# Kernel tuning notes

Hardware: AMD Instinct MI355X
Metric: run time of the kernel (lower is better)

Reference implementation:

```python
import jax, jax.numpy as jnp
import numpy as np

B, T, D, HEADS = 4, 2048, 2048, 16  # math requires T == D


def setup_inputs() -> dict:
    key = jax.random.key(0)
    k1, k2, k3 = jax.random.split(key, 3)
    scale = 1.0 / np.sqrt(D)
    x = jax.random.normal(k1, (B, T, D), dtype=jnp.float32)
    w_qk = jax.random.normal(k2, (2 * D, D), dtype=jnp.float32) * scale
    w_dense = jax.random.normal(k3, (D, D), dtype=jnp.float32) * scale
    b_dense = jnp.zeros((D,), dtype=jnp.float32)
    return {"x": x, "w_qk": w_qk, "w_dense": w_dense, "b_dense": b_dense}


def reference(x, w_qk, w_dense, b_dense):
    b, t, d = x.shape
    h = HEADS
    vh = d // h
    # to_q_k: Linear(d, 2d, bias=False); chunk into k0, v
    kv = jnp.einsum('btd,ed->bte', x, w_qk)          # [b,t,2d]
    k0, v = kv[..., :d], kv[..., d:]                 # each [b,t,d]
    scale_factor = 1.0 / jnp.sqrt(jnp.asarray(d * (d - 1) / 2, dtype=x.dtype))
    # k = k0.transpose(1,2) -> [b,d,t]; scores = k @ v^T -> [b,d,t] (t==d)
    s = jnp.einsum('bmi,bjm->bij', k0, v) * scale_factor   # [b,d,t]
    a = jax.nn.softmax(s, axis=-1)
    q = jnp.einsum('bit,btd->bid', a, v)             # [b,d,d]
    # q.transpose(0,1).chunk(h, dim=0) -> stack(dim=1) -> transpose(1,2) -> reshape
    qt = jnp.swapaxes(q, 0, 1)                       # [d, b, d]
    stk = qt.reshape(h, vh, b, d)                    # h chunks of [vh,b,d]
    stk = jnp.transpose(stk, (1, 0, 2, 3))           # stack(dim=1): [vh,h,b,d]
    stk = jnp.transpose(stk, (0, 2, 1, 3))           # transpose(1,2): [vh,b,h,d]
    out = stk.reshape(b, t, d)
    # dropout in eval mode == identity; to_dense Linear
    return jnp.einsum('btd,ed->bte', out, w_dense) + b_dense
```

## Files before the change

### kernel.cpp

```cpp
#include <hip/hip_runtime.h>
#include <stdint.h>
#include <math.h>


typedef __bf16 bf16x8 __attribute__((ext_vector_type(8)));
typedef float  f32x4  __attribute__((ext_vector_type(4)));

__device__ __forceinline__ float bf2f(uint16_t u) {
  union { uint32_t i; float f; } c; c.i = ((uint32_t)u) << 16; return c.f;
}
__device__ __forceinline__ uint16_t f2bf(float f) {
  union { float f; uint32_t i; } c; c.f = f;
  uint32_t i = c.i;
  return (uint16_t)((i + 0x7fffu + ((i >> 16) & 1u)) >> 16);
}

__device__ __forceinline__ void gll16(const void* g, void* l) {
  __builtin_amdgcn_global_load_lds((const __attribute__((address_space(1))) void*)g,
                                   (__attribute__((address_space(3))) void*)l,
                                   16, 0, 0);
}

#define NX4 4194304u
#define NW4 2097152u
#define ND4 1048576u
__global__ __launch_bounds__(256) void k_cast_all(
    const float* __restrict__ x, const float* __restrict__ wqk,
    const float* __restrict__ wd, uint16_t* __restrict__ dst) {
  uint32_t i = blockIdx.x * 256 + threadIdx.x;
  float4 v;
  if (i < NX4)            v = reinterpret_cast<const float4*>(x)[i];
  else if (i < NX4 + NW4) v = reinterpret_cast<const float4*>(wqk)[i - NX4];
  else                    v = reinterpret_cast<const float4*>(wd)[i - NX4 - NW4];
  ushort4 o;
  o.x = f2bf(v.x); o.y = f2bf(v.y); o.z = f2bf(v.z); o.w = f2bf(v.w);
  reinterpret_cast<ushort4*>(dst)[i] = o;
}

__device__ __forceinline__ void gemm_core(
    const uint16_t* a0, const uint16_t* a1, const uint16_t* a2, const uint16_t* a3,
    const uint16_t* b0, const uint16_t* b1, const uint16_t* b2, const uint16_t* b3,
    uint16_t* As, uint16_t* Bs, int K, f32x4 acc[4][4])
{
  const int tid = threadIdx.x;
  const int w = tid >> 6, l = tid & 63;
  const int wm = (w >> 1) * 64, wn = (w & 1) * 64;
  const int frow = l & 15, fkc = l >> 4;
  const int xr = frow & 7;
  const int off0 = ((0 * 4 + fkc) ^ xr) * 8;
  const int off1 = ((1 * 4 + fkc) ^ xr) * 8;
  uint16_t* lA0 = As + 0 * 2048 + w * 512;
  uint16_t* lA1 = As + 1 * 2048 + w * 512;
  uint16_t* lA2 = As + 2 * 2048 + w * 512;
  uint16_t* lA3 = As + 3 * 2048 + w * 512;
  uint16_t* lB0 = Bs + 0 * 2048 + w * 512;
  uint16_t* lB1 = Bs + 1 * 2048 + w * 512;
  uint16_t* lB2 = Bs + 2 * 2048 + w * 512;
  uint16_t* lB3 = Bs + 3 * 2048 + w * 512;
  for (int kb = 0; kb < K; kb += 64) {
    __syncthreads();
    gll16(a0, lA0); gll16(a1, lA1); gll16(a2, lA2); gll16(a3, lA3);
    gll16(b0, lB0); gll16(b1, lB1); gll16(b2, lB2); gll16(b3, lB3);
    a0 += 64; a1 += 64; a2 += 64; a3 += 64;
    b0 += 64; b1 += 64; b2 += 64; b3 += 64;
    __syncthreads();
#pragma unroll
    for (int h = 0; h < 2; ++h) {
      const int off = h ? off1 : off0;
      bf16x8 af[4], bfv[4];
#pragma unroll
      for (int mi = 0; mi < 4; ++mi)
        af[mi] = *reinterpret_cast<const bf16x8*>(&As[(wm + mi * 16 + frow) * 64 + off]);
#pragma unroll
      for (int ni = 0; ni < 4; ++ni)
        bfv[ni] = *reinterpret_cast<const bf16x8*>(&Bs[(wn + ni * 16 + frow) * 64 + off]);
#pragma unroll
      for (int mi = 0; mi < 4; ++mi)
#pragma unroll
        for (int ni = 0; ni < 4; ++ni)
          acc[mi][ni] = __builtin_amdgcn_mfma_f32_16x16x32_bf16(af[mi], bfv[ni], acc[mi][ni], 0, 0, 0);
    }
  }
}

__device__ __forceinline__ const uint16_t* stage_ptr(
    const uint16_t* base, int tile_row0, int c, int lda) {
  const int tid = threadIdx.x;
  const int r3 = tid >> 3;
  const int ko = (((tid & 7) ^ (r3 & 7)) * 8);
  return base + (size_t)(tile_row0 + c * 32 + r3) * lda + ko;
}

__global__ __launch_bounds__(256) void k_gemm_kv(
    const uint16_t* __restrict__ W,
    const uint16_t* __restrict__ X,
    uint16_t* __restrict__ k0T,
    uint16_t* __restrict__ vT)
{
  __shared__ uint16_t As[8192], Bs[8192];
  const int bm = blockIdx.y, bn = blockIdx.x;
  f32x4 acc[4][4];
#pragma unroll
  for (int i = 0; i < 4; ++i)
#pragma unroll
    for (int j = 0; j < 4; ++j) acc[i][j] = (f32x4){0.f, 0.f, 0.f, 0.f};
  gemm_core(stage_ptr(W, bm * 128, 0, 2048), stage_ptr(W, bm * 128, 1, 2048),
            stage_ptr(W, bm * 128, 2, 2048), stage_ptr(W, bm * 128, 3, 2048),
            stage_ptr(X, bn * 128, 0, 2048), stage_ptr(X, bn * 128, 1, 2048),
            stage_ptr(X, bn * 128, 2, 2048), stage_ptr(X, bn * 128, 3, 2048),
            As, Bs, 2048, acc);
  const int tid = threadIdx.x;
  const int w = tid >> 6, l = tid & 63;
  const int wm = (w >> 1) * 64, wn = (w & 1) * 64;
  const int cr = (l >> 4) * 4, cc = l & 15;
  uint16_t* Cb = (bm < 16) ? (k0T + (size_t)bm * 128 * 8192)
                           : (vT + (size_t)(bm - 16) * 128 * 8192);
#pragma unroll
  for (int mi = 0; mi < 4; ++mi)
#pragma unroll
    for (int ni = 0; ni < 4; ++ni)
#pragma unroll
      for (int g = 0; g < 4; ++g) {
        int lr = wm + mi * 16 + cr + g;
        int bt = bn * 128 + wn + ni * 16 + cc;
        Cb[(size_t)lr * 8192 + bt] = f2bf(acc[mi][ni][g]);
      }
}

__global__ __launch_bounds__(256) void k_gemm_bt(
    const uint16_t* __restrict__ A, int lda, long sA,
    const uint16_t* __restrict__ B, int ldb, long sB,
    uint16_t* __restrict__ C, int ldc, long sC,
    int K, float scale)
{
  __shared__ uint16_t As[8192], Bs[8192];
  const int z = blockIdx.z;
  A += (size_t)z * sA; B += (size_t)z * sB; C += (size_t)z * sC;
  const int bm = blockIdx.y, bn = blockIdx.x;
  f32x4 acc[4][4];
#pragma unroll
  for (int i = 0; i < 4; ++i)
#pragma unroll
    for (int j = 0; j < 4; ++j) acc[i][j] = (f32x4){0.f, 0.f, 0.f, 0.f};
  gemm_core(stage_ptr(A, bm * 128, 0, lda), stage_ptr(A, bm * 128, 1, lda),
            stage_ptr(A, bm * 128, 2, lda), stage_ptr(A, bm * 128, 3, lda),
            stage_ptr(B, bn * 128, 0, ldb), stage_ptr(B, bn * 128, 1, ldb),
            stage_ptr(B, bn * 128, 2, ldb), stage_ptr(B, bn * 128, 3, ldb),
            As, Bs, K, acc);
  const int tid = threadIdx.x;
  const int w = tid >> 6, l = tid & 63;
  const int wm = (w >> 1) * 64, wn = (w & 1) * 64;
  const int cr = (l >> 4) * 4, cc = l & 15;
#pragma unroll
  for (int mi = 0; mi < 4; ++mi)
#pragma unroll
    for (int ni = 0; ni < 4; ++ni)
#pragma unroll
      for (int g = 0; g < 4; ++g) {
        int grow = bm * 128 + wm + mi * 16 + cr + g;
        int gcol = bn * 128 + wn + ni * 16 + cc;
        C[(size_t)grow * ldc + gcol] = f2bf(acc[mi][ni][g] * scale);
      }
}

__device__ __forceinline__ size_t qrow_off(int rr) {
  int bp = rr >> 11, tp = rr & 2047;
  int bi = (tp >> 4) & 3;
  int i  = (tp & 15) * 128 + bp * 32 + (tp >> 6);
  return ((size_t)bi * 2048 + (size_t)i) * 2048;
}

__global__ __launch_bounds__(256) void k_gemm_out(
    const uint16_t* __restrict__ Q,
    const uint16_t* __restrict__ W,
    const float*    __restrict__ bias,
    float*          __restrict__ Out)
{
  __shared__ uint16_t As[8192], Bs[8192];
  const int tid = threadIdx.x;
  const int bm = blockIdx.y, bn = blockIdx.x;
  const int r3 = tid >> 3;
  const int ko = (((tid & 7) ^ (r3 & 7)) * 8);
  const uint16_t* a0 = Q + qrow_off(bm * 128 + 0 * 32 + r3) + ko;
  const uint16_t* a1 = Q + qrow_off(bm * 128 + 1 * 32 + r3) + ko;
  const uint16_t* a2 = Q + qrow_off(bm * 128 + 2 * 32 + r3) + ko;
  const uint16_t* a3 = Q + qrow_off(bm * 128 + 3 * 32 + r3) + ko;
  f32x4 acc[4][4];
#pragma unroll
  for (int i = 0; i < 4; ++i)
#pragma unroll
    for (int j = 0; j < 4; ++j) acc[i][j] = (f32x4){0.f, 0.f, 0.f, 0.f};
  gemm_core(a0, a1, a2, a3,
            stage_ptr(W, bn * 128, 0, 2048), stage_ptr(W, bn * 128, 1, 2048),
            stage_ptr(W, bn * 128, 2, 2048), stage_ptr(W, bn * 128, 3, 2048),
            As, Bs, 2048, acc);
  const int w = tid >> 6, l = tid & 63;
  const int wm = (w >> 1) * 64, wn = (w & 1) * 64;
  const int cr = (l >> 4) * 4, cc = l & 15;
#pragma unroll
  for (int mi = 0; mi < 4; ++mi)
#pragma unroll
    for (int ni = 0; ni < 4; ++ni)
#pragma unroll
      for (int g = 0; g < 4; ++g) {
        int grow = bm * 128 + wm + mi * 16 + cr + g;
        int gcol = bn * 128 + wn + ni * 16 + cc;
        Out[(size_t)grow * 2048 + gcol] = acc[mi][ni][g] + bias[gcol];
      }
}

__global__ __launch_bounds__(256) void k_transpose(
    const uint16_t* __restrict__ src, uint16_t* __restrict__ dst)
{
  __shared__ uint16_t tile[64][65];
  const int tid = threadIdx.x;
  const int bx = blockIdx.x;
  const int by = blockIdx.y;
  const int cu = tid & 31, r0 = tid >> 5;
#pragma unroll
  for (int p = 0; p < 8; ++p) {
    int r = p * 8 + r0;
    uint32_t v = *reinterpret_cast<const uint32_t*>(
        &src[(size_t)(by * 64 + r) * 8192 + bx * 64 + cu * 2]);
    tile[r][cu * 2]     = (uint16_t)(v & 0xffffu);
    tile[r][cu * 2 + 1] = (uint16_t)(v >> 16);
  }
  __syncthreads();
#pragma unroll
  for (int p = 0; p < 8; ++p) {
    int r = p * 8 + r0;
    uint32_t lo = tile[cu * 2][r], hi = tile[cu * 2 + 1][r];
    *reinterpret_cast<uint32_t*>(
        &dst[(size_t)(bx * 64 + r) * 2048 + by * 64 + cu * 2]) = lo | (hi << 16);
  }
}

__global__ __launch_bounds__(256) void k_softmax(uint16_t* __restrict__ s)
{
  uint16_t* p = s + (size_t)blockIdx.x * 2048;
  const int tid = threadIdx.x;
  uint4 raw = reinterpret_cast<const uint4*>(p)[tid];
  uint32_t u[4] = {raw.x, raw.y, raw.z, raw.w};
  float x[8];
#pragma unroll
  for (int i = 0; i < 4; ++i) {
    x[2 * i]     = bf2f((uint16_t)(u[i] & 0xffffu));
    x[2 * i + 1] = bf2f((uint16_t)(u[i] >> 16));
  }
  float m = x[0];
#pragma unroll
  for (int i = 1; i < 8; ++i) m = fmaxf(m, x[i]);
#pragma unroll
  for (int o = 32; o; o >>= 1) m = fmaxf(m, __shfl_xor(m, o, 64));
  __shared__ float redm[4], reds[4];
  if ((tid & 63) == 0) redm[tid >> 6] = m;
  __syncthreads();
  m = fmaxf(fmaxf(redm[0], redm[1]), fmaxf(redm[2], redm[3]));
  float sum = 0.f;
#pragma unroll
  for (int i = 0; i < 8; ++i) { x[i] = __expf(x[i] - m); sum += x[i]; }
#pragma unroll
  for (int o = 32; o; o >>= 1) sum += __shfl_xor(sum, o, 64);
  if ((tid & 63) == 0) reds[tid >> 6] = sum;
  __syncthreads();
  sum = reds[0] + reds[1] + reds[2] + reds[3];
  float inv = 1.0f / sum;
  uint32_t ou[4];
#pragma unroll
  for (int i = 0; i < 4; ++i) {
    uint32_t lo = f2bf(x[2 * i] * inv);
    uint32_t hi = f2bf(x[2 * i + 1] * inv);
    ou[i] = lo | (hi << 16);
  }
  reinterpret_cast<uint4*>(p)[tid] = make_uint4(ou[0], ou[1], ou[2], ou[3]);
}

extern "C" void kernel_launch(void* const* d_in, const int* in_sizes, int n_in,
                              void* d_out, int out_size, void* d_ws, size_t ws_size,
                              hipStream_t stream) {
  const float* x       = (const float*)d_in[0];
  const float* w_qk    = (const float*)d_in[1];
  const float* w_dense = (const float*)d_in[2];
  const float* b_dense = (const float*)d_in[3];
  float* out = (float*)d_out;

  const size_t NX = 4ull * 2048 * 2048;
  const size_t NW = 4096ull * 2048;
  const size_t ND = 2048ull * 2048;

  uint16_t* xb   = (uint16_t*)d_ws;
  uint16_t* wqkb = xb + NX;
  uint16_t* wdb  = wqkb + NW;
  uint16_t* k0T  = wdb + ND;
  uint16_t* vT   = k0T + NX;
  uint16_t* qb   = xb;
  uint16_t* Vn   = (uint16_t*)d_out;
  uint16_t* sb   = Vn + NX;

  const float scale = (float)(1.0 / sqrt(0.5 * 2048.0 * 2047.0));

  k_cast_all<<<dim3((NX4 + NW4 + ND4) / 256), 256, 0, stream>>>(x, w_qk, w_dense, xb);

  k_gemm_kv<<<dim3(64, 32), 256, 0, stream>>>(wqkb, xb, k0T, vT);
  k_transpose<<<dim3(128, 32), 256, 0, stream>>>(vT, Vn);
  k_gemm_bt<<<dim3(16, 16, 4), 256, 0, stream>>>(
      k0T, 8192, 2048L, Vn, 2048, 2048L * 2048L, sb, 2048, 2048L * 2048L, 2048, scale);
  k_softmax<<<dim3(8192), 256, 0, stream>>>(sb);
  k_gemm_bt<<<dim3(16, 16, 4), 256, 0, stream>>>(
      sb, 2048, 2048L * 2048L, vT, 8192, 2048L, qb, 2048, 2048L * 2048L, 2048, 1.0f);
  k_gemm_out<<<dim3(16, 64), 256, 0, stream>>>(qb, wdb, b_dense, out);
}
```

Before: 575.9 us.

## Replace direct global-to-LDS loads with register-prefetched double staging in GEMM core

```diff
diff --git a/kernel.cpp b/kernel.cpp
--- a/kernel.cpp
+++ b/kernel.cpp
@@ -13,12 +13,6 @@
   union { float f; uint32_t i; } c; c.f = f;
   uint32_t i = c.i;
   return (uint16_t)((i + 0x7fffu + ((i >> 16) & 1u)) >> 16);
-}
-
-__device__ __forceinline__ void gll16(const void* g, void* l) {
-  __builtin_amdgcn_global_load_lds((const __attribute__((address_space(1))) void*)g,
-                                   (__attribute__((address_space(3))) void*)l,
-                                   16, 0, 0);
 }
 
 #define NX4 4194304u
@@ -37,7 +31,15 @@
   reinterpret_cast<ushort4*>(dst)[i] = o;
 }
 
-__device__ __forceinline__ void gemm_core(
+__device__ __forceinline__ const uint16_t* stage_ptr(
+    const uint16_t* base, int tile_row0, int c, int lda) {
+  const int tid = threadIdx.x;
+  const int r3 = tid >> 3;
+  const int ko = (((tid & 7) ^ (r3 & 7)) * 8);
+  return base + (size_t)(tile_row0 + c * 32 + r3) * lda + ko;
+}
+
+__device__ __forceinline__ void gemm_core_reg(
     const uint16_t* a0, const uint16_t* a1, const uint16_t* a2, const uint16_t* a3,
     const uint16_t* b0, const uint16_t* b1, const uint16_t* b2, const uint16_t* b3,
     uint16_t* As, uint16_t* Bs, int K, f32x4 acc[4][4])
@@ -47,23 +49,41 @@
   const int wm = (w >> 1) * 64, wn = (w & 1) * 64;
   const int frow = l & 15, fkc = l >> 4;
   const int xr = frow & 7;
-  const int off0 = ((0 * 4 + fkc) ^ xr) * 8;
-  const int off1 = ((1 * 4 + fkc) ^ xr) * 8;
-  uint16_t* lA0 = As + 0 * 2048 + w * 512;
-  uint16_t* lA1 = As + 1 * 2048 + w * 512;
-  uint16_t* lA2 = As + 2 * 2048 + w * 512;
-  uint16_t* lA3 = As + 3 * 2048 + w * 512;
-  uint16_t* lB0 = Bs + 0 * 2048 + w * 512;
-  uint16_t* lB1 = Bs + 1 * 2048 + w * 512;
-  uint16_t* lB2 = Bs + 2 * 2048 + w * 512;
-  uint16_t* lB3 = Bs + 3 * 2048 + w * 512;
+  const int off0 = (fkc ^ xr) * 8;
+  const int off1 = ((4 + fkc) ^ xr) * 8;
+  const int lw = (tid >> 3) * 64 + (tid & 7) * 8;
+
+  uint4 ra0, ra1, ra2, ra3, rb0, rb1, rb2, rb3;
+  ra0 = *reinterpret_cast<const uint4*>(a0); a0 += 64;
+  ra1 = *reinterpret_cast<const uint4*>(a1); a1 += 64;
+  ra2 = *reinterpret_cast<const uint4*>(a2); a2 += 64;
+  ra3 = *reinterpret_cast<const uint4*>(a3); a3 += 64;
+  rb0 = *reinterpret_cast<const uint4*>(b0); b0 += 64;
+  rb1 = *reinterpret_cast<const uint4*>(b1); b1 += 64;
+  rb2 = *reinterpret_cast<const uint4*>(b2); b2 += 64;
+  rb3 = *reinterpret_cast<const uint4*>(b3); b3 += 64;
+
   for (int kb = 0; kb < K; kb += 64) {
     __syncthreads();
-    gll16(a0, lA0); gll16(a1, lA1); gll16(a2, lA2); gll16(a3, lA3);
-    gll16(b0, lB0); gll16(b1, lB1); gll16(b2, lB2); gll16(b3, lB3);
-    a0 += 64; a1 += 64; a2 += 64; a3 += 64;
-    b0 += 64; b1 += 64; b2 += 64; b3 += 64;
+    *reinterpret_cast<uint4*>(&As[lw])        = ra0;
+    *reinterpret_cast<uint4*>(&As[lw + 2048]) = ra1;
+    *reinterpret_cast<uint4*>(&As[lw + 4096]) = ra2;
+    *reinterpret_cast<uint4*>(&As[lw + 6144]) = ra3;
+    *reinterpret_cast<uint4*>(&Bs[lw])        = rb0;
+    *reinterpret_cast<uint4*>(&Bs[lw + 2048]) = rb1;
+    *reinterpret_cast<uint4*>(&Bs[lw + 4096]) = rb2;
+    *reinterpret_cast<uint4*>(&Bs[lw + 6144]) = rb3;
     __syncthreads();
+    if (kb + 64 < K) {
+      ra0 = *reinterpret_cast<const uint4*>(a0); a0 += 64;
+      ra1 = *reinterpret_cast<const uint4*>(a1); a1 += 64;
+      ra2 = *reinterpret_cast<const uint4*>(a2); a2 += 64;
+      ra3 = *reinterpret_cast<const uint4*>(a3); a3 += 64;
+      rb0 = *reinterpret_cast<const uint4*>(b0); b0 += 64;
+      rb1 = *reinterpret_cast<const uint4*>(b1); b1 += 64;
+      rb2 = *reinterpret_cast<const uint4*>(b2); b2 += 64;
+      rb3 = *reinterpret_cast<const uint4*>(b3); b3 += 64;
+    }
 #pragma unroll
     for (int h = 0; h < 2; ++h) {
       const int off = h ? off1 : off0;
@@ -81,14 +101,6 @@
           acc[mi][ni] = __builtin_amdgcn_mfma_f32_16x16x32_bf16(af[mi], bfv[ni], acc[mi][ni], 0, 0, 0);
     }
   }
-}
-
-__device__ __forceinline__ const uint16_t* stage_ptr(
-    const uint16_t* base, int tile_row0, int c, int lda) {
-  const int tid = threadIdx.x;
-  const int r3 = tid >> 3;
-  const int ko = (((tid & 7) ^ (r3 & 7)) * 8);
-  return base + (size_t)(tile_row0 + c * 32 + r3) * lda + ko;
 }
 
 __global__ __launch_bounds__(256) void k_gemm_kv(
@@ -104,11 +116,11 @@
   for (int i = 0; i < 4; ++i)
 #pragma unroll
     for (int j = 0; j < 4; ++j) acc[i][j] = (f32x4){0.f, 0.f, 0.f, 0.f};
-  gemm_core(stage_ptr(W, bm * 128, 0, 2048), stage_ptr(W, bm * 128, 1, 2048),
-            stage_ptr(W, bm * 128, 2, 2048), stage_ptr(W, bm * 128, 3, 2048),
-            stage_ptr(X, bn * 128, 0, 2048), stage_ptr(X, bn * 128, 1, 2048),
-            stage_ptr(X, bn * 128, 2, 2048), stage_ptr(X, bn * 128, 3, 2048),
-            As, Bs, 2048, acc);
+  gemm_core_reg(stage_ptr(W, bm * 128, 0, 2048), stage_ptr(W, bm * 128, 1, 2048),
+                stage_ptr(W, bm * 128, 2, 2048), stage_ptr(W, bm * 128, 3, 2048),
+                stage_ptr(X, bn * 128, 0, 2048), stage_ptr(X, bn * 128, 1, 2048),
+                stage_ptr(X, bn * 128, 2, 2048), stage_ptr(X, bn * 128, 3, 2048),
+                As, Bs, 2048, acc);
   const int tid = threadIdx.x;
   const int w = tid >> 6, l = tid & 63;
   const int wm = (w >> 1) * 64, wn = (w & 1) * 64;
@@ -142,11 +154,11 @@
   for (int i = 0; i < 4; ++i)
 #pragma unroll
     for (int j = 0; j < 4; ++j) acc[i][j] = (f32x4){0.f, 0.f, 0.f, 0.f};
-  gemm_core(stage_ptr(A, bm * 128, 0, lda), stage_ptr(A, bm * 128, 1, lda),
-            stage_ptr(A, bm * 128, 2, lda), stage_ptr(A, bm * 128, 3, lda),
-            stage_ptr(B, bn * 128, 0, ldb), stage_ptr(B, bn * 128, 1, ldb),
-            stage_ptr(B, bn * 128, 2, ldb), stage_ptr(B, bn * 128, 3, ldb),
-            As, Bs, K, acc);
+  gemm_core_reg(stage_ptr(A, bm * 128, 0, lda), stage_ptr(A, bm * 128, 1, lda),
+                stage_ptr(A, bm * 128, 2, lda), stage_ptr(A, bm * 128, 3, lda),
+                stage_ptr(B, bn * 128, 0, ldb), stage_ptr(B, bn * 128, 1, ldb),
+                stage_ptr(B, bn * 128, 2, ldb), stage_ptr(B, bn * 128, 3, ldb),
+                As, Bs, K, acc);
   const int tid = threadIdx.x;
   const int w = tid >> 6, l = tid & 63;
   const int wm = (w >> 1) * 64, wn = (w & 1) * 64;
@@ -180,7 +192,7 @@
   const int tid = threadIdx.x;
   const int bm = blockIdx.y, bn = blockIdx.x;
   const int r3 = tid >> 3;
-  const int ko = (((tid & 7) ^ (r3 & 7)) * 8);
+  const int ko = ((tid & 7) ^ (r3 & 7)) * 8;
   const uint16_t* a0 = Q + qrow_off(bm * 128 + 0 * 32 + r3) + ko;
   const uint16_t* a1 = Q + qrow_off(bm * 128 + 1 * 32 + r3) + ko;
   const uint16_t* a2 = Q + qrow_off(bm * 128 + 2 * 32 + r3) + ko;
@@ -190,10 +202,10 @@
   for (int i = 0; i < 4; ++i)
 #pragma unroll
     for (int j = 0; j < 4; ++j) acc[i][j] = (f32x4){0.f, 0.f, 0.f, 0.f};
-  gemm_core(a0, a1, a2, a3,
-            stage_ptr(W, bn * 128, 0, 2048), stage_ptr(W, bn * 128, 1, 2048),
-            stage_ptr(W, bn * 128, 2, 2048), stage_ptr(W, bn * 128, 3, 2048),
-            As, Bs, 2048, acc);
+  gemm_core_reg(a0, a1, a2, a3,
+                stage_ptr(W, bn * 128, 0, 2048), stage_ptr(W, bn * 128, 1, 2048),
+                stage_ptr(W, bn * 128, 2, 2048), stage_ptr(W, bn * 128, 3, 2048),
+                As, Bs, 2048, acc);
   const int w = tid >> 6, l = tid & 63;
   const int wm = (w >> 1) * 64, wn = (w & 1) * 64;
   const int cr = (l >> 4) * 4, cc = l & 15;
```

Measured after the change: 539.3 us. 6.4% less time.
